# Performance work log

Measured on AMD Instinct MI355X. Metric: run time of the kernel, lower is better.

The kernel has to match this reference:

```python
import jax, jax.numpy as jnp
import numpy as np

NUM_INPUTS = 784
NUM_OUTPUTS = 784
WIDTH_POW = 10
WIDTH = 2 ** WIDTH_POW          # 1024
HALF = WIDTH // 2               # 512
DEPTH = 8
BDEPTH = 10
DEGREE = 2
BATCH = 4096

# knots from the source: tensor([-256..256]) / 32
_KNOTS = np.array([-256., -128., -64., -32., -16., -8., -4., -2., -1., 0.,
                   1., 2., 4., 8., 16., 32., 64., 128., 256.], dtype=np.float32) / 32.0
# clamped (open) knot vector: repeat endpoints `degree` times
_T = np.concatenate([np.full(DEGREE, _KNOTS[0]), _KNOTS, np.full(DEGREE, _KNOTS[-1])]).astype(np.float32)
SPLINE_DIM = len(_T) - DEGREE - 1  # 20 basis functions


def _bspline_basis(x):
    """Cox-de Boor B-spline basis, vectorized over all elements of x.
    Returns basis of shape x.shape + (SPLINE_DIM,)."""
    t = jnp.asarray(_T)
    x = jnp.clip(x, _T[0], _T[-1] - 1e-6)  # clamp to knot span (eval domain)
    xe = x[..., None]
    B = ((xe >= t[:-1]) & (xe < t[1:])).astype(x.dtype)  # degree-0 indicators
    for k in range(1, DEGREE + 1):
        tj, tjk = t[:-(k + 1)], t[k:-1]
        tj1, tjk1 = t[1:-k], t[k + 1:]
        d1, d2 = tjk - tj, tjk1 - tj1
        w1 = jnp.where(d1 > 0, (xe - tj) / jnp.where(d1 > 0, d1, 1.0), 0.0)
        w2 = jnp.where(d2 > 0, (tjk1 - xe) / jnp.where(d2 > 0, d2, 1.0), 0.0)
        B = w1 * B[..., :-1] + w2 * B[..., 1:]
    return B  # [..., SPLINE_DIM]


def _butterfly(X, params):
    """OrthogonalButterfly.forward. params: [HALF, BDEPTH]. X: [B, WIDTH]."""
    Bsz = X.shape[0]
    for d in range(BDEPTH):
        theta = params[:, d]
        c, s = jnp.cos(theta), jnp.sin(theta)
        X0, X1 = X[:, :HALF], X[:, HALF:]
        n0 = X0 * c + X1 * s
        n1 = -X0 * s + X1 * c
        # perm[i] = i//2 (even) / i//2 + half (odd) == interleave halves
        X = jnp.stack([n0, n1], axis=2).reshape(Bsz, WIDTH)
    return X


def _forward(X, butterfly_params, spline_coefs):
    Bsz = X.shape[0]
    X = jnp.concatenate([X, jnp.zeros((Bsz, WIDTH - NUM_INPUTS), X.dtype)], axis=1)
    for i in range(DEPTH):
        X = _butterfly(X, butterfly_params[i])
        if i != DEPTH - 1:
            # ReversibleActivation: X0 += spline(X1), per-column spline coefs
            X0, X1 = X[:, :HALF], X[:, HALF:]
            act = jnp.einsum('bwd,wd->bw', _bspline_basis(X1), spline_coefs[i])
            X = jnp.concatenate([X0 + act, X1], axis=1)
    return X[:, :NUM_OUTPUTS]


def setup_inputs() -> dict:
    key = jax.random.key(0)
    k1, k2, k3 = jax.random.split(key, 3)
    X = jax.random.normal(k1, (BATCH, NUM_INPUTS), dtype=jnp.float32)
    butterfly_params = jax.random.uniform(k2, (DEPTH, HALF, BDEPTH), dtype=jnp.float32) * (2.0 * np.pi)
    spline_coefs = jax.random.uniform(k3, (DEPTH - 1, HALF, SPLINE_DIM), dtype=jnp.float32) * 0.2 - 0.1
    return {"X": X, "butterfly_params": butterfly_params, "spline_coefs": spline_coefs}


def reference(X, butterfly_params, spline_coefs):
    return _forward(X, butterfly_params, spline_coefs)
```

## Files before the change

kernel.cpp:

```cpp
#include <hip/hip_runtime.h>

#define NIN 784
#define WIDTH 1024
#define HALF 512
#define DEPTH 8
#define BDEPTH 10
#define BATCH 4096
#define SPLINE_DIM 20
#define NQ 18

typedef __attribute__((ext_vector_type(2))) float f32x2;

__device__ float d_T[23] = {
  -8.f, -8.f, -8.f, -4.f, -2.f, -1.f, -0.5f, -0.25f, -0.125f, -0.0625f,
  -0.03125f, 0.f, 0.03125f, 0.0625f, 0.125f, 0.25f, 0.5f, 1.f, 2.f, 4.f,
  8.f, 8.f, 8.f };

__global__ void prep_kernel(const float* __restrict__ bp,
                            const float* __restrict__ sc,
                            float2* __restrict__ cs,
                            float4* __restrict__ qt) {
  int gid = blockIdx.x * 256 + threadIdx.x;
  if (gid < DEPTH * BDEPTH * 1024) {
    int slot = gid & 1023;
    int d = (gid >> 10) % BDEPTH;
    int i = gid / (BDEPTH * 1024);
    int n = 0;
#pragma unroll
    for (int b = 0; b < 10; ++b) {
      int src = b - d; if (src < 0) src += 10;
      n |= ((slot >> src) & 1) << b;
    }
    int pj = n & 511;
    float theta = bp[(i * HALF + pj) * BDEPTH + d];
    float c = cosf(theta), s = sinf(theta);
    float2 val = make_float2(c, (n & 512) ? -s : s);
    int off;
    if (d < 4) off = i * 10240 + d * 1024 + slot;
    else {
      int p = (d - 4) >> 1, sub = (d - 4) & 1;
      off = i * 10240 + 4096 + p * 2048 + slot * 2 + sub;
    }
    cs[off] = val;
  }
  int gid2 = gid - DEPTH * BDEPTH * 1024;
  if (gid2 >= 0 && gid2 < (DEPTH - 1) * NQ * HALF) {
    int w = gid2 & 511;
    int mi = (gid2 >> 9) % NQ;
    int i = gid2 / (NQ * HALF);
    int m = mi + 2;
    const float* cf = sc + (i * HALF + w) * SPLINE_DIM;
    double c0 = cf[mi], c1 = cf[mi + 1], c2 = cf[mi + 2];
    double tm1 = d_T[m - 1], tm = d_T[m], tp1 = d_T[m + 1], tp2 = d_T[m + 2];
    double h = tp1 - tm;
    double us[3] = { 0.0, 0.5 * h, 0.75 * h };
    double y[3];
#pragma unroll
    for (int k = 0; k < 3; ++k) {
      double x = tm + us[k];
      double left1 = x - tm, right1 = tp1 - x, left2 = x - tm1, right2 = tp2 - x;
      double inv1 = 1.0 / (tp1 - tm);
      double N0 = right1 * inv1, N1 = left1 * inv1;
      double temp0 = N0 / (tp1 - tm1);
      double B0 = right1 * temp0;
      double saved = left2 * temp0;
      double temp1 = N1 / (tp2 - tm);
      double B1 = right2 * temp1 + saved;
      double B2 = left1 * temp1;
      y[k] = c0 * B0 + c1 * B1 + c2 * B2;
    }
    double d1 = y[1] - y[0], d2 = y[2] - y[0];
    double u1 = us[1], u2 = us[2];
    double det = u1 * u2 * (u2 - u1);
    double Bq = (d1 * u2 * u2 - d2 * u1 * u1) / det;
    double Cq = (d2 * u1 - d1 * u2) / det;
    qt[gid2] = make_float4((float)y[0], (float)Bq, (float)Cq, (float)tm);
  }
}

template <int M>
__device__ __forceinline__ float shfx(float x) {
  if constexpr (M == 1)
    return __int_as_float(__builtin_amdgcn_mov_dpp(__float_as_int(x), 0xB1, 0xF, 0xF, true));
  else if constexpr (M == 2)
    return __int_as_float(__builtin_amdgcn_mov_dpp(__float_as_int(x), 0x4E, 0xF, 0xF, true));
  else if constexpr (M == 4)
    return __int_as_float(__builtin_amdgcn_ds_swizzle(__float_as_int(x), 0x101F));
  else if constexpr (M == 8)
    return __int_as_float(__builtin_amdgcn_ds_swizzle(__float_as_int(x), 0x201F));
  else if constexpr (M == 16)
    return __int_as_float(__builtin_amdgcn_ds_swizzle(__float_as_int(x), 0x401F));
  else
    return __shfl_xor(x, 32, 64);
}

__device__ __forceinline__ float qspline(float x, const float4* __restrict__ qL, int w) {
  x = fminf(fmaxf(x, -8.0f), 7.9999990f);
  float ax = fabsf(x);
  unsigned bits = __float_as_uint(ax);
  int e = (int)(bits >> 23) - 127;
  int ce = e + ((bits & 0x7fffffu) ? 1 : 0);
  int m = (x > 0.f) ? (17 + e) : (5 - ce);
  m = (ax < 0.03125f) ? ((x < 0.f) ? 10 : 11) : m;
  float4 qc = qL[(m - 2) * HALF + w];
  float u = x - qc.w;
  return fmaf(u, fmaf(u, qc.z, qc.y), qc.x);
}

typedef __attribute__((address_space(3))) unsigned int lds_u32;
typedef __attribute__((address_space(1))) const unsigned int glb_u32;

__device__ __forceinline__ void stage_async(const float2* __restrict__ src,
                                            float2* dst, int wv) {
#pragma unroll
  for (int k = 0; k < 10; ++k) {
    int seg = k * 8 + wv;
    const char* g = (const char*)src + seg * 1024 + (threadIdx.x & 63) * 16;
    char* l = (char*)dst + seg * 1024;
    __builtin_amdgcn_global_load_lds((glb_u32*)g, (lds_u32*)l, 16, 0, 0);
  }
}

#define CSTEPL(dd) do {                                                       \
    const int _mr = 8 >> (dd);                                                \
    _Pragma("unroll") for (int r = 0; r < 16; ++r)                            \
      if ((r & _mr) == 0) {                                                   \
        float2 v = cur[(dd) * 1024 + r * 64 + lane];                          \
        f32x2 a = st[r], b2 = st[r + _mr];                                    \
        f32x2 vc = {v.x, v.x}, vs = {v.y, v.y};                               \
        st[r]       = __builtin_elementwise_fma(a, vc, b2 * vs);              \
        st[r + _mr] = __builtin_elementwise_fma(b2, vc, -(a * vs));           \
      }                                                                       \
  } while (0)

#define LPAIR(p, M1, M2) do {                                                 \
    const float4* _pp = (const float4*)(cur + 4096 + (p) * 2048);             \
    _Pragma("unroll") for (int r = 0; r < 16; ++r) {                          \
      float4 v = _pp[r * 64 + lane];                                          \
      f32x2 q1 = { shfx<M1>(st[r].x), shfx<M1>(st[r].y) };                    \
      st[r] = __builtin_elementwise_fma(st[r], (f32x2){v.x, v.x},             \
                                        q1 * (f32x2){v.y, v.y});              \
      f32x2 q2 = { shfx<M2>(st[r].x), shfx<M2>(st[r].y) };                    \
      st[r] = __builtin_elementwise_fma(st[r], (f32x2){v.z, v.z},             \
                                        q2 * (f32x2){v.w, v.w});              \
    }                                                                         \
  } while (0)

__global__ __launch_bounds__(512, 1) void fwd_kernel(
    const float* __restrict__ X, const float2* __restrict__ cs,
    const float4* __restrict__ qt, float* __restrict__ out) {
  __shared__ float2 bufA[10240];
  __shared__ float2 bufB[10240];
  int tid = threadIdx.x;
  int lane = tid & 63;
  int wv = tid >> 6;
  int row0 = blockIdx.x * 16 + wv * 2;

  const float* x0p = X + (long)row0 * NIN;
  const float* x1p = X + (long)(row0 + 1) * NIN;
  f32x2 st[16];
#pragma unroll
  for (int r = 0; r < 16; ++r) {
    int w = r * 64 + lane;
    bool in = (w < NIN);
    st[r] = (f32x2){ in ? x0p[w] : 0.f, in ? x1p[w] : 0.f };
  }

  stage_async(cs, bufA, wv);

#pragma unroll 1
  for (int i = 0; i < DEPTH; ++i) {
    const float2* cur = (i & 1) ? bufB : bufA;
    float2* nxt = (i & 1) ? bufA : bufB;

    __syncthreads();
    stage_async(cs + ((i + 1) & 7) * 10240, nxt, wv);
    asm volatile("s_waitcnt vmcnt(10)" ::: "memory");
    __syncthreads();

    CSTEPL(0);
    CSTEPL(1);
    CSTEPL(2);
    CSTEPL(3);
    LPAIR(0, 32, 16);
    LPAIR(1, 8, 4);
    LPAIR(2, 2, 1);

    if (i != DEPTH - 1) {
      const float4* qL = qt + i * (NQ * HALF);
#pragma unroll
      for (int r = 8; r < 16; ++r) {
        int w = ((r - 8) << 6) | lane;
        st[r - 8].x += qspline(st[r].x, qL, w);
        st[r - 8].y += qspline(st[r].y, qL, w);
      }
    }
  }

  float* o0 = out + (long)row0 * NIN;
  float* o1 = out + (long)(row0 + 1) * NIN;
#pragma unroll
  for (int r = 0; r < 13; ++r) {
    int w = r * 64 + lane;
    if (w < NIN) { o0[w] = st[r].x; o1[w] = st[r].y; }
  }
}

extern "C" void kernel_launch(void* const* d_in, const int* in_sizes, int n_in,
                              void* d_out, int out_size, void* d_ws, size_t ws_size,
                              hipStream_t stream) {
  const float* X  = (const float*)d_in[0];
  const float* bp = (const float*)d_in[1];
  const float* sc = (const float*)d_in[2];
  float* out = (float*)d_out;

  float2* cs = (float2*)d_ws;
  float4* qt = (float4*)((char*)d_ws + DEPTH * BDEPTH * 1024 * sizeof(float2));

  int prep_threads = DEPTH * BDEPTH * 1024 + (DEPTH - 1) * NQ * HALF;
  prep_kernel<<<(prep_threads + 255) / 256, 256, 0, stream>>>(bp, sc, cs, qt);
  fwd_kernel<<<BATCH / 16, 512, 0, stream>>>(X, cs, qt, out);
}
```

Before: 66.35 us.

## Compact register-level rotation tables and use DPP/permlane swaps for cross-lane shuffles

Repacks the coefficients for the first four butterfly stages so each thread loads only the 8 rotation pairs it needs per stage, as paired float4s, instead of 16 float2 reads per stage where half are unused. This shrinks the per-layer LDS table from 10240 to 8192 float2 and cuts async global-to-LDS staging from 10 to 8 segments. The cross-lane exchanges for distances 8, 16 and 32 move from ds_swizzle/shfl to DPP row_ror and permlane16/32 swap builtins when available, avoiding the LDS crossbar. The prep kernel's index mapping has to match the new consumption order exactly, so a mistake there would produce wrong results.

```diff
diff --git a/kernel.cpp b/kernel.cpp
--- a/kernel.cpp
+++ b/kernel.cpp
@@ -8,6 +8,7 @@
 #define BATCH 4096
 #define SPLINE_DIM 20
 #define NQ 18
+#define LSTRIDE 8192
 
 typedef __attribute__((ext_vector_type(2))) float f32x2;
 
@@ -35,13 +36,23 @@
     float theta = bp[(i * HALF + pj) * BDEPTH + d];
     float c = cosf(theta), s = sinf(theta);
     float2 val = make_float2(c, (n & 512) ? -s : s);
-    int off;
-    if (d < 4) off = i * 10240 + d * 1024 + slot;
-    else {
+    long base = (long)i * LSTRIDE;
+    if (d < 4) {
+      int r = slot >> 6, lane = slot & 63;
+      int mr = 8 >> d;
+      if ((r & mr) == 0) {
+        int q;
+        if (d == 0)      q = r;
+        else if (d == 1) q = (r & 3) | ((r >> 3) << 2);
+        else if (d == 2) q = ((r >> 2) << 1) | (r & 1);
+        else             q = r >> 1;
+        int tbl = d >> 1, sub = d & 1;
+        cs[base + tbl * 1024 + (q * 64 + lane) * 2 + sub] = val;
+      }
+    } else {
       int p = (d - 4) >> 1, sub = (d - 4) & 1;
-      off = i * 10240 + 4096 + p * 2048 + slot * 2 + sub;
-    }
-    cs[off] = val;
+      cs[base + 2048 + p * 2048 + slot * 2 + sub] = val;
+    }
   }
   int gid2 = gid - DEPTH * BDEPTH * 1024;
   if (gid2 >= 0 && gid2 < (DEPTH - 1) * NQ * HALF) {
@@ -79,7 +90,7 @@
 }
 
 template <int M>
-__device__ __forceinline__ float shfx(float x) {
+__device__ __forceinline__ float shfx(float x, int lane) {
   if constexpr (M == 1)
     return __int_as_float(__builtin_amdgcn_mov_dpp(__float_as_int(x), 0xB1, 0xF, 0xF, true));
   else if constexpr (M == 2)
@@ -87,11 +98,22 @@
   else if constexpr (M == 4)
     return __int_as_float(__builtin_amdgcn_ds_swizzle(__float_as_int(x), 0x101F));
   else if constexpr (M == 8)
-    return __int_as_float(__builtin_amdgcn_ds_swizzle(__float_as_int(x), 0x201F));
-  else if constexpr (M == 16)
+    return __int_as_float(__builtin_amdgcn_mov_dpp(__float_as_int(x), 0x128, 0xF, 0xF, true));
+  else if constexpr (M == 16) {
+#if __has_builtin(__builtin_amdgcn_permlane16_swap)
+    auto pr = __builtin_amdgcn_permlane16_swap(__float_as_uint(x), __float_as_uint(x), false, false);
+    return __uint_as_float((lane & 16) ? pr[0] : pr[1]);
+#else
     return __int_as_float(__builtin_amdgcn_ds_swizzle(__float_as_int(x), 0x401F));
-  else
+#endif
+  } else {
+#if __has_builtin(__builtin_amdgcn_permlane32_swap)
+    auto pr = __builtin_amdgcn_permlane32_swap(__float_as_uint(x), __float_as_uint(x), false, false);
+    return __uint_as_float((lane & 32) ? pr[0] : pr[1]);
+#else
     return __shfl_xor(x, 32, 64);
+#endif
+  }
 }
 
 __device__ __forceinline__ float qspline(float x, const float4* __restrict__ qL, int w) {
@@ -113,7 +135,7 @@
 __device__ __forceinline__ void stage_async(const float2* __restrict__ src,
                                             float2* dst, int wv) {
 #pragma unroll
-  for (int k = 0; k < 10; ++k) {
+  for (int k = 0; k < 8; ++k) {
     int seg = k * 8 + wv;
     const char* g = (const char*)src + seg * 1024 + (threadIdx.x & 63) * 16;
     char* l = (char*)dst + seg * 1024;
@@ -121,26 +143,21 @@
   }
 }
 
-#define CSTEPL(dd) do {                                                       \
-    const int _mr = 8 >> (dd);                                                \
-    _Pragma("unroll") for (int r = 0; r < 16; ++r)                            \
-      if ((r & _mr) == 0) {                                                   \
-        float2 v = cur[(dd) * 1024 + r * 64 + lane];                          \
-        f32x2 a = st[r], b2 = st[r + _mr];                                    \
-        f32x2 vc = {v.x, v.x}, vs = {v.y, v.y};                               \
-        st[r]       = __builtin_elementwise_fma(a, vc, b2 * vs);              \
-        st[r + _mr] = __builtin_elementwise_fma(b2, vc, -(a * vs));           \
-      }                                                                       \
+#define ROT(rz, rp, cc, ss) do {                                              \
+    f32x2 _a = st[rz], _b = st[rp];                                           \
+    f32x2 _vc = {cc, cc}, _vs = {ss, ss};                                     \
+    st[rz] = __builtin_elementwise_fma(_a, _vc, _b * _vs);                    \
+    st[rp] = __builtin_elementwise_fma(_b, _vc, -(_a * _vs));                 \
   } while (0)
 
 #define LPAIR(p, M1, M2) do {                                                 \
-    const float4* _pp = (const float4*)(cur + 4096 + (p) * 2048);             \
+    const float4* _pp = (const float4*)(cur + 2048 + (p) * 2048);             \
     _Pragma("unroll") for (int r = 0; r < 16; ++r) {                          \
       float4 v = _pp[r * 64 + lane];                                          \
-      f32x2 q1 = { shfx<M1>(st[r].x), shfx<M1>(st[r].y) };                    \
+      f32x2 q1 = { shfx<M1>(st[r].x, lane), shfx<M1>(st[r].y, lane) };        \
       st[r] = __builtin_elementwise_fma(st[r], (f32x2){v.x, v.x},             \
                                         q1 * (f32x2){v.y, v.y});              \
-      f32x2 q2 = { shfx<M2>(st[r].x), shfx<M2>(st[r].y) };                    \
+      f32x2 q2 = { shfx<M2>(st[r].x, lane), shfx<M2>(st[r].y, lane) };        \
       st[r] = __builtin_elementwise_fma(st[r], (f32x2){v.z, v.z},             \
                                         q2 * (f32x2){v.w, v.w});              \
     }                                                                         \
@@ -149,8 +166,8 @@
 __global__ __launch_bounds__(512, 1) void fwd_kernel(
     const float* __restrict__ X, const float2* __restrict__ cs,
     const float4* __restrict__ qt, float* __restrict__ out) {
-  __shared__ float2 bufA[10240];
-  __shared__ float2 bufB[10240];
+  __shared__ float2 bufA[LSTRIDE];
+  __shared__ float2 bufB[LSTRIDE];
   int tid = threadIdx.x;
   int lane = tid & 63;
   int wv = tid >> 6;
@@ -174,14 +191,39 @@
     float2* nxt = (i & 1) ? bufA : bufB;
 
     __syncthreads();
-    stage_async(cs + ((i + 1) & 7) * 10240, nxt, wv);
-    asm volatile("s_waitcnt vmcnt(10)" ::: "memory");
+    stage_async(cs + ((i + 1) & 7) * LSTRIDE, nxt, wv);
+    asm volatile("s_waitcnt vmcnt(8)" ::: "memory");
     __syncthreads();
 
-    CSTEPL(0);
-    CSTEPL(1);
-    CSTEPL(2);
-    CSTEPL(3);
+    {
+      const float4* cp = (const float4*)cur;
+      float4 V[8];
+#pragma unroll
+      for (int q = 0; q < 8; ++q) V[q] = cp[q * 64 + lane];
+#pragma unroll
+      for (int q = 0; q < 8; ++q) ROT(q, q + 8, V[q].x, V[q].y);
+#pragma unroll
+      for (int q = 0; q < 8; ++q) {
+        const int rz = (q < 4) ? q : q + 4;
+        ROT(rz, rz + 4, V[q].z, V[q].w);
+      }
+    }
+    {
+      const float4* cp = (const float4*)(cur + 1024);
+      float4 V[8];
+#pragma unroll
+      for (int q = 0; q < 8; ++q) V[q] = cp[q * 64 + lane];
+#pragma unroll
+      for (int q = 0; q < 8; ++q) {
+        const int rz = ((q >> 1) << 2) | (q & 1);
+        ROT(rz, rz + 2, V[q].x, V[q].y);
+      }
+#pragma unroll
+      for (int q = 0; q < 8; ++q) {
+        const int rz = 2 * q;
+        ROT(rz, rz + 1, V[q].z, V[q].w);
+      }
+    }
     LPAIR(0, 32, 16);
     LPAIR(1, 8, 4);
     LPAIR(2, 2, 1);
@@ -215,7 +257,7 @@
   float* out = (float*)d_out;
 
   float2* cs = (float2*)d_ws;
-  float4* qt = (float4*)((char*)d_ws + DEPTH * BDEPTH * 1024 * sizeof(float2));
+  float4* qt = (float4*)((char*)d_ws + DEPTH * LSTRIDE * sizeof(float2));
 
   int prep_threads = DEPTH * BDEPTH * 1024 + (DEPTH - 1) * NQ * HALF;
   prep_kernel<<<(prep_threads + 255) / 256, 256, 0, stream>>>(bp, sc, cs, qt);
```

After: 61.81 us. 6.8% less time.
